# Optimization experiments

Measured on AMD Instinct MI355X. Metric: run time of the kernel, lower is better.

The kernel has to match this reference:

```python
import jax, jax.numpy as jnp
import numpy as np

N_NODES = 100000
D = 128        # input_dim / feature dim
H = 128        # hidden_dim
O = 64         # output_dim (classes)
B = 4096       # batch of seed nodes
S = 16         # sample_num (neighbor fan-out)


def setup_inputs() -> dict:
    key = jax.random.key(0)
    k1, k2, k3, k4, k5, k6, k7 = jax.random.split(key, 7)
    nodes = jax.random.randint(k1, (B,), 0, N_NODES)
    neighbors_1 = jax.random.randint(k2, (B, S), 0, N_NODES)
    neighbors_2 = jax.random.randint(k3, (B * S, S), 0, N_NODES)
    node_features = jax.random.normal(k4, (N_NODES, D), dtype=jnp.float32)
    # xavier-uniform, no bias (matches nn.Linear weight layout [out, in])
    def xavier(k, out_d, in_d):
        lim = float(np.sqrt(6.0 / (in_d + out_d)))
        return jax.random.uniform(k, (out_d, in_d), jnp.float32, -lim, lim)
    W1 = xavier(k5, H, 2 * D)   # fc_layer_1 (concat=True -> input_dim*2)
    W2 = xavier(k6, H, 2 * D)   # fc_layer_2
    Wo = xavier(k7, O, H)       # output_layer
    return {"nodes": nodes, "neighbors_1": neighbors_1, "neighbors_2": neighbors_2,
            "node_features": node_features, "W1": W1, "W2": W2, "Wo": Wo}


def reference(nodes, neighbors_1, neighbors_2, node_features, W1, W2, Wo):
    # Level-1 neighbor node list (flattened samples of the seed nodes)
    neighs_nodes_1 = neighbors_1.reshape(-1)                 # [B*S]
    features_origin = node_features[nodes]                   # [B, D]
    features_1 = node_features[neighs_nodes_1]               # [B*S, D]

    # aggregator_1: mean over sampled 2-hop neighbors of each level-1 node
    agg_feat_1 = node_features[neighbors_2].mean(axis=1)     # [B*S, D]
    agg_feat_1 = jnp.concatenate([features_1, agg_feat_1], axis=-1)  # [B*S, 2D]
    agg_embed_1 = jax.nn.relu(agg_feat_1 @ W1.T)             # [B*S, H] (unused downstream, as in original)

    # aggregator_2: mean over sampled 1-hop neighbors of each seed node
    agg_feat_2 = node_features[neighbors_1].mean(axis=1)     # [B, D]
    agg_feat_2 = jnp.concatenate([features_origin, agg_feat_2], axis=-1)  # [B, 2D]
    agg_embed_2 = jax.nn.relu(agg_feat_2 @ W2.T)             # [B, H]

    logits = agg_embed_2 @ Wo.T                              # [B, O]
    return jax.nn.softmax(logits, axis=-1)
```

## Files before the change

### kernel.cpp

```cpp
#include <hip/hip_runtime.h>


constexpr int D = 128;
constexpr int H = 128;
constexpr int O = 64;
constexpr int S = 16;
constexpr int NB = 4096;

__global__ __launch_bounds__(64) void k_gather(
    const int* __restrict__ nodes,
    const int* __restrict__ neigh,
    const float* __restrict__ nf,
    float* __restrict__ cat)
{
    const int seed = blockIdx.x;
    const int lane = threadIdx.x;
    const int d4   = lane & 31;
    const int sub  = lane >> 5;
    const float4* nf4 = reinterpret_cast<const float4*>(nf);

    const int4* nbp = reinterpret_cast<const int4*>(neigh + (size_t)seed * S + sub * 8);
    const int4 n0 = nbp[0], n1 = nbp[1];
    const int ids[8] = {n0.x, n0.y, n0.z, n0.w, n1.x, n1.y, n1.z, n1.w};

    float4 sum = make_float4(0.f, 0.f, 0.f, 0.f);
    #pragma unroll
    for (int s = 0; s < 8; ++s) {
        const float4 v = nf4[(size_t)ids[s] * (D / 4) + d4];
        sum.x += v.x; sum.y += v.y; sum.z += v.z; sum.w += v.w;
    }
    float4 tot;
    tot.x = sum.x + __shfl_xor(sum.x, 32);
    tot.y = sum.y + __shfl_xor(sum.y, 32);
    tot.z = sum.z + __shfl_xor(sum.z, 32);
    tot.w = sum.w + __shfl_xor(sum.w, 32);

    float4* o4 = reinterpret_cast<float4*>(cat + (size_t)seed * (2 * D));
    if (sub == 0) {
        o4[d4] = nf4[(size_t)nodes[seed] * (D / 4) + d4];
    } else {
        o4[32 + d4] = make_float4(tot.x * 0.0625f, tot.y * 0.0625f,
                                  tot.z * 0.0625f, tot.w * 0.0625f);
    }
}

constexpr int SPB = 8;
constexpr int KP  = 32;

__global__ __launch_bounds__(256, 2) void k_mlp(
    const float* __restrict__ cat,
    const float* __restrict__ W2,
    const float* __restrict__ Wo,
    float* __restrict__ out)
{
    __shared__ float catl[SPB][2 * D];
    __shared__ float w2l[2][H][KP];
    __shared__ float wol[O][D];
    __shared__ float hl[SPB][H];

    const int t  = threadIdx.x;
    const int s0 = blockIdx.x * SPB;

    float4 pv[4];
    #pragma unroll
    for (int i = 0; i < 4; ++i) {
        const int idx = t + i * 256, row = idx >> 3, c4 = idx & 7;
        pv[i] = *reinterpret_cast<const float4*>(W2 + (size_t)row * (2 * D) + c4 * 4);
    }
    float4 cv0, cv1;
    {
        const float4* cg = reinterpret_cast<const float4*>(cat + (size_t)s0 * 2 * D);
        cv0 = cg[t]; cv1 = cg[t + 256];
    }
    float4 wv[8];
    #pragma unroll
    for (int i = 0; i < 8; ++i)
        wv[i] = reinterpret_cast<const float4*>(Wo)[t + i * 256];

    {
        float4* cl = reinterpret_cast<float4*>(&catl[0][0]);
        cl[t] = cv0; cl[t + 256] = cv1;
    }
    #pragma unroll
    for (int i = 0; i < 8; ++i) {
        const int idx = t + i * 256, c = idx >> 5, k4 = idx & 31;
        *reinterpret_cast<float4*>(&wol[c][((k4 & 24) | ((k4 ^ c) & 7)) << 2]) = wv[i];
    }

    const int j0 = t & 63;
    const int sg = t >> 6;
    const int sA = sg * 2, sB = sA + 1;
    const int swz = j0 & 7;
    float acc00 = 0.f, acc01 = 0.f, acc10 = 0.f, acc11 = 0.f;

    for (int p = 0; p < 8; ++p) {
        const int cur = p & 1;
        #pragma unroll
        for (int i = 0; i < 4; ++i) {
            const int idx = t + i * 256, row = idx >> 3, c4 = idx & 7;
            *reinterpret_cast<float4*>(&w2l[cur][row][(c4 ^ (row & 7)) << 2]) = pv[i];
        }
        __syncthreads();
        if (p < 7) {
            #pragma unroll
            for (int i = 0; i < 4; ++i) {
                const int idx = t + i * 256, row = idx >> 3, c4 = idx & 7;
                pv[i] = *reinterpret_cast<const float4*>(
                    W2 + (size_t)row * (2 * D) + (p + 1) * KP + c4 * 4);
            }
        }
        #pragma unroll
        for (int k4 = 0; k4 < 8; ++k4) {
            const float4 wA = *reinterpret_cast<const float4*>(&w2l[cur][j0][(k4 ^ swz) << 2]);
            const float4 wB = *reinterpret_cast<const float4*>(&w2l[cur][j0 + 64][(k4 ^ swz) << 2]);
            const float4 cA = *reinterpret_cast<const float4*>(&catl[sA][p * KP + k4 * 4]);
            const float4 cB = *reinterpret_cast<const float4*>(&catl[sB][p * KP + k4 * 4]);
            acc00 = fmaf(wA.x, cA.x, acc00); acc00 = fmaf(wA.y, cA.y, acc00);
            acc00 = fmaf(wA.z, cA.z, acc00); acc00 = fmaf(wA.w, cA.w, acc00);
            acc01 = fmaf(wA.x, cB.x, acc01); acc01 = fmaf(wA.y, cB.y, acc01);
            acc01 = fmaf(wA.z, cB.z, acc01); acc01 = fmaf(wA.w, cB.w, acc01);
            acc10 = fmaf(wB.x, cA.x, acc10); acc10 = fmaf(wB.y, cA.y, acc10);
            acc10 = fmaf(wB.z, cA.z, acc10); acc10 = fmaf(wB.w, cA.w, acc10);
            acc11 = fmaf(wB.x, cB.x, acc11); acc11 = fmaf(wB.y, cB.y, acc11);
            acc11 = fmaf(wB.z, cB.z, acc11); acc11 = fmaf(wB.w, cB.w, acc11);
        }
        __syncthreads();
    }

    hl[sA][j0]      = acc00 > 0.f ? acc00 : 0.f;
    hl[sB][j0]      = acc01 > 0.f ? acc01 : 0.f;
    hl[sA][j0 + 64] = acc10 > 0.f ? acc10 : 0.f;
    hl[sB][j0 + 64] = acc11 > 0.f ? acc11 : 0.f;
    __syncthreads();

    {
        const int c = t & 63;
        const int cswz = c & 7;
        float a0 = 0.f, a1 = 0.f;
        #pragma unroll
        for (int k4 = 0; k4 < 32; ++k4) {
            const float4 w = *reinterpret_cast<const float4*>(
                &wol[c][((k4 & 24) | ((k4 ^ cswz) & 7)) << 2]);
            const float4 h0 = *reinterpret_cast<const float4*>(&hl[sA][k4 * 4]);
            const float4 h1 = *reinterpret_cast<const float4*>(&hl[sB][k4 * 4]);
            a0 = fmaf(w.x, h0.x, a0); a0 = fmaf(w.y, h0.y, a0);
            a0 = fmaf(w.z, h0.z, a0); a0 = fmaf(w.w, h0.w, a0);
            a1 = fmaf(w.x, h1.x, a1); a1 = fmaf(w.y, h1.y, a1);
            a1 = fmaf(w.z, h1.z, a1); a1 = fmaf(w.w, h1.w, a1);
        }
        float m0 = a0, m1 = a1;
        #pragma unroll
        for (int off = 32; off >= 1; off >>= 1) {
            m0 = fmaxf(m0, __shfl_xor(m0, off));
            m1 = fmaxf(m1, __shfl_xor(m1, off));
        }
        const float e0 = __expf(a0 - m0), e1 = __expf(a1 - m1);
        float z0 = e0, z1 = e1;
        #pragma unroll
        for (int off = 32; off >= 1; off >>= 1) {
            z0 += __shfl_xor(z0, off);
            z1 += __shfl_xor(z1, off);
        }
        out[(size_t)(s0 + sA) * O + c] = e0 / z0;
        out[(size_t)(s0 + sB) * O + c] = e1 / z1;
    }
}

extern "C" void kernel_launch(void* const* d_in, const int* in_sizes, int n_in,
                              void* d_out, int out_size, void* d_ws, size_t ws_size,
                              hipStream_t stream) {
    const int*   nodes         = (const int*)d_in[0];
    const int*   neighbors_1   = (const int*)d_in[1];
    const float* node_features = (const float*)d_in[3];
    const float* W2            = (const float*)d_in[5];
    const float* Wo            = (const float*)d_in[6];
    float*       out           = (float*)d_out;
    float*       cat           = (float*)d_ws;

    k_gather<<<NB, 64, 0, stream>>>(nodes, neighbors_1, node_features, cat);
    k_mlp<<<NB / SPB, 256, 0, stream>>>(cat, W2, Wo, out);
}
```

Baseline: 126.6 us.

## Fuse neighbor gather into MLP kernel, writing concat features directly to LDS

Merges the gather kernel and the MLP kernel into a single launch. Each wave gathers and averages neighbor features for two seeds and writes the concatenated row straight into shared memory, so the global workspace write and reread of the concat buffer go away, along with one kernel launch. In exchange, gather latency is now exposed inside the MLP blocks, with fewer blocks (512) in flight to hide the random-access loads.

Measured after the change: 122.6 us. 3.1% less time.

```diff
diff --git a/kernel.cpp b/kernel.cpp
--- a/kernel.cpp
+++ b/kernel.cpp
@@ -6,49 +6,13 @@
 constexpr int O = 64;
 constexpr int S = 16;
 constexpr int NB = 4096;
+constexpr int SPB = 8;
+constexpr int KP  = 32;
 
-__global__ __launch_bounds__(64) void k_gather(
+__global__ __launch_bounds__(256, 2) void sage_fused(
     const int* __restrict__ nodes,
     const int* __restrict__ neigh,
     const float* __restrict__ nf,
-    float* __restrict__ cat)
-{
-    const int seed = blockIdx.x;
-    const int lane = threadIdx.x;
-    const int d4   = lane & 31;
-    const int sub  = lane >> 5;
-    const float4* nf4 = reinterpret_cast<const float4*>(nf);
-
-    const int4* nbp = reinterpret_cast<const int4*>(neigh + (size_t)seed * S + sub * 8);
-    const int4 n0 = nbp[0], n1 = nbp[1];
-    const int ids[8] = {n0.x, n0.y, n0.z, n0.w, n1.x, n1.y, n1.z, n1.w};
-
-    float4 sum = make_float4(0.f, 0.f, 0.f, 0.f);
-    #pragma unroll
-    for (int s = 0; s < 8; ++s) {
-        const float4 v = nf4[(size_t)ids[s] * (D / 4) + d4];
-        sum.x += v.x; sum.y += v.y; sum.z += v.z; sum.w += v.w;
-    }
-    float4 tot;
-    tot.x = sum.x + __shfl_xor(sum.x, 32);
-    tot.y = sum.y + __shfl_xor(sum.y, 32);
-    tot.z = sum.z + __shfl_xor(sum.z, 32);
-    tot.w = sum.w + __shfl_xor(sum.w, 32);
-
-    float4* o4 = reinterpret_cast<float4*>(cat + (size_t)seed * (2 * D));
-    if (sub == 0) {
-        o4[d4] = nf4[(size_t)nodes[seed] * (D / 4) + d4];
-    } else {
-        o4[32 + d4] = make_float4(tot.x * 0.0625f, tot.y * 0.0625f,
-                                  tot.z * 0.0625f, tot.w * 0.0625f);
-    }
-}
-
-constexpr int SPB = 8;
-constexpr int KP  = 32;
-
-__global__ __launch_bounds__(256, 2) void k_mlp(
-    const float* __restrict__ cat,
     const float* __restrict__ W2,
     const float* __restrict__ Wo,
     float* __restrict__ out)
@@ -67,29 +31,69 @@
         const int idx = t + i * 256, row = idx >> 3, c4 = idx & 7;
         pv[i] = *reinterpret_cast<const float4*>(W2 + (size_t)row * (2 * D) + c4 * 4);
     }
-    float4 cv0, cv1;
+
     {
-        const float4* cg = reinterpret_cast<const float4*>(cat + (size_t)s0 * 2 * D);
-        cv0 = cg[t]; cv1 = cg[t + 256];
+        const int lane = t & 63;
+        const int wv_  = t >> 6;
+        const int d4   = lane & 31;
+        const int sub  = lane >> 5;
+        const float4* nf4 = reinterpret_cast<const float4*>(nf);
+
+        int ids[2][8];
+        #pragma unroll
+        for (int si = 0; si < 2; ++si) {
+            const int4* nbp = reinterpret_cast<const int4*>(
+                neigh + (size_t)(s0 + 2 * wv_ + si) * S + sub * 8);
+            const int4 a = nbp[0], b = nbp[1];
+            ids[si][0] = a.x; ids[si][1] = a.y; ids[si][2] = a.z; ids[si][3] = a.w;
+            ids[si][4] = b.x; ids[si][5] = b.y; ids[si][6] = b.z; ids[si][7] = b.w;
+        }
+        float4 sum[2] = {make_float4(0.f, 0.f, 0.f, 0.f),
+                         make_float4(0.f, 0.f, 0.f, 0.f)};
+        float4 orgv[2];
+        #pragma unroll
+        for (int si = 0; si < 2; ++si)
+            orgv[si] = nf4[(size_t)nodes[s0 + 2 * wv_ + si] * (D / 4) + d4];
+        #pragma unroll
+        for (int k = 0; k < 8; ++k) {
+            #pragma unroll
+            for (int si = 0; si < 2; ++si) {
+                const float4 v = nf4[(size_t)ids[si][k] * (D / 4) + d4];
+                sum[si].x += v.x; sum[si].y += v.y;
+                sum[si].z += v.z; sum[si].w += v.w;
+            }
+        }
+        #pragma unroll
+        for (int si = 0; si < 2; ++si) {
+            float4 tot;
+            tot.x = sum[si].x + __shfl_xor(sum[si].x, 32);
+            tot.y = sum[si].y + __shfl_xor(sum[si].y, 32);
+            tot.z = sum[si].z + __shfl_xor(sum[si].z, 32);
+            tot.w = sum[si].w + __shfl_xor(sum[si].w, 32);
+            const int s = 2 * wv_ + si;
+            if (sub == 0) {
+                *reinterpret_cast<float4*>(&catl[s][4 * d4]) = orgv[si];
+            } else {
+                *reinterpret_cast<float4*>(&catl[s][D + 4 * d4]) =
+                    make_float4(tot.x * 0.0625f, tot.y * 0.0625f,
+                                tot.z * 0.0625f, tot.w * 0.0625f);
+            }
+        }
     }
+
     float4 wv[8];
     #pragma unroll
     for (int i = 0; i < 8; ++i)
         wv[i] = reinterpret_cast<const float4*>(Wo)[t + i * 256];
-
-    {
-        float4* cl = reinterpret_cast<float4*>(&catl[0][0]);
-        cl[t] = cv0; cl[t + 256] = cv1;
-    }
     #pragma unroll
     for (int i = 0; i < 8; ++i) {
         const int idx = t + i * 256, c = idx >> 5, k4 = idx & 31;
         *reinterpret_cast<float4*>(&wol[c][((k4 & 24) | ((k4 ^ c) & 7)) << 2]) = wv[i];
     }
 
-    const int j0 = t & 63;
-    const int sg = t >> 6;
-    const int sA = sg * 2, sB = sA + 1;
+    const int j0  = t & 63;
+    const int sg  = t >> 6;
+    const int sA  = sg * 2, sB = sA + 1;
     const int swz = j0 & 7;
     float acc00 = 0.f, acc01 = 0.f, acc10 = 0.f, acc11 = 0.f;
 
@@ -175,8 +179,7 @@
     const float* W2            = (const float*)d_in[5];
     const float* Wo            = (const float*)d_in[6];
     float*       out           = (float*)d_out;
-    float*       cat           = (float*)d_ws;
 
-    k_gather<<<NB, 64, 0, stream>>>(nodes, neighbors_1, node_features, cat);
-    k_mlp<<<NB / SPB, 256, 0, stream>>>(cat, W2, Wo, out);
+    sage_fused<<<NB / SPB, 256, 0, stream>>>(
+        nodes, neighbors_1, node_features, W2, Wo, out);
 }
```
